# Kernel optimization log

Measured on AMD Instinct MI355X. Metric: run time of the kernel, lower is better.

## Reference

```python
import jax, jax.numpy as jnp
import numpy as np
import math

NUM_HEADS = 8

def setup_inputs() -> dict:
    key = jax.random.key(0)
    ks = jax.random.split(key, 5)
    b, h, w, c = 4, 128, 128, 256
    x = jax.random.normal(ks[0], (b, h, w, c), dtype=jnp.float32)
    scale = 1.0 / math.sqrt(c)  # keep weights reasonably scaled (kaiming-like)
    Wq = jax.random.normal(ks[1], (c, c), dtype=jnp.float32) * scale
    Wk = jax.random.normal(ks[2], (c, c), dtype=jnp.float32) * scale
    Wv = jax.random.normal(ks[3], (c, c), dtype=jnp.float32) * scale
    Wout = jax.random.normal(ks[4], (c, c), dtype=jnp.float32) * scale
    return {"x": x, "Wq": Wq, "Wk": Wk, "Wv": Wv, "Wout": Wout}

def reference(x, Wq, Wk, Wv, Wout):
    b, h, w, c = x.shape
    hw = h * w
    heads = NUM_HEADS
    dh = c // heads
    xs = x.reshape(b, hw, c)
    q = xs @ Wq  # (b, hw, c)
    k = xs @ Wk
    v = xs @ Wv

    def split_heads(t):
        # (b, hw, c) -> (b, c, hw) -> (b, heads, dh, hw)
        return t.transpose(0, 2, 1).reshape(b, heads, dh, hw)

    q = split_heads(q)
    k = split_heads(k)
    v = split_heads(v)
    # L2-normalize along the feature (hw) axis; original has no epsilon
    q = q / jnp.linalg.norm(q, axis=-1, keepdims=True)
    k = k / jnp.linalg.norm(k, axis=-1, keepdims=True)
    d_k = q.shape[-1]  # = hw
    attn = jnp.einsum('bhcd,bhed->bhce', q, k) / math.sqrt(d_k)  # (b,heads,dh,dh)
    attn = jax.nn.softmax(attn, axis=-1)
    vals = jnp.einsum('bhce,bhed->bhcd', attn, v)  # (b,heads,dh,hw)
    vals = vals.transpose(0, 3, 1, 2).reshape(b, hw, c)
    out = (vals @ Wout).reshape(b, h, w, c)
    return out
```

## Files before the change

### kernel.cpp

```cpp
#include <hip/hip_runtime.h>


#define B_   4
#define HW_  16384
#define C_   256

typedef __attribute__((ext_vector_type(8))) short short8;
typedef __attribute__((ext_vector_type(4))) float floatx4;

__device__ __forceinline__ unsigned short f2bf(float f) {
  unsigned u = __builtin_bit_cast(unsigned, f);
  u += 0x7FFFu + ((u >> 16) & 1u);
  return (unsigned short)(u >> 16);
}

__device__ __forceinline__ void gl_lds16(const unsigned short* g, unsigned short* l) {
  __builtin_amdgcn_global_load_lds(
      (const __attribute__((address_space(1))) unsigned int*)g,
      (__attribute__((address_space(3))) unsigned int*)l, 16, 0, 0);
}

__global__ __launch_bounds__(256) void k_cast_tr(const float* __restrict__ x,
                                                 unsigned short* __restrict__ xb,
                                                 unsigned short* __restrict__ xT) {
  __shared__ unsigned short lds[64][72];
  int bid = blockIdx.x;
  int ct = bid & 3;
  int pt = (bid >> 2) & 255;
  int b  = bid >> 10;
  int t = threadIdx.x;
  const float* src = x + ((size_t)(b * HW_ + pt * 64)) * C_ + ct * 64;
#pragma unroll
  for (int e = 0; e < 4; e++) {
    int lin = t + e * 256;
    int p = lin >> 4, c4 = lin & 15;
    float4 v = *(const float4*)(src + (size_t)p * C_ + c4 * 4);
    ushort4 h;
    h.x = f2bf(v.x); h.y = f2bf(v.y); h.z = f2bf(v.z); h.w = f2bf(v.w);
    *(ushort4*)(xb + ((size_t)(b * HW_ + pt * 64 + p)) * C_ + ct * 64 + c4 * 4) = h;
    lds[c4 * 4 + 0][p] = h.x;
    lds[c4 * 4 + 1][p] = h.y;
    lds[c4 * 4 + 2][p] = h.z;
    lds[c4 * 4 + 3][p] = h.w;
  }
  __syncthreads();
#pragma unroll
  for (int e = 0; e < 4; e++) {
    int lin = t + e * 256;
    int c = lin >> 4, p4 = lin & 15;
    ushort4 h;
    h.x = lds[c][p4 * 4 + 0];
    h.y = lds[c][p4 * 4 + 1];
    h.z = lds[c][p4 * 4 + 2];
    h.w = lds[c][p4 * 4 + 3];
    *(ushort4*)(xT + ((size_t)(b * C_ + ct * 64 + c)) * HW_ + pt * 64 + p4 * 4) = h;
  }
}

template <int NST>
__device__ __forceinline__ void nt_loop(const unsigned short* Ab, int lda,
                                        const unsigned short* Bb, int ldb,
                                        unsigned short* At, unsigned short* Bt,
                                        floatx4 acc[4][4]) {
  int t = threadIdx.x;
  int lane = t & 63, w = t >> 6;
  int wm = w >> 1, wn = w & 1;
  int l8 = lane >> 3, l7 = lane & 7;
  int srcoct = l7 ^ l8;
  int l15 = lane & 15, l4 = lane >> 4;
  for (int s = 0; s < NST; s++) {
#pragma unroll
    for (int i = 0; i < 4; i++) {
      int gi = w * 4 + i;
      int row = gi * 8 + l8;
      gl_lds16(Ab + (size_t)row * lda + s * 64 + srcoct * 8, At + gi * 512);
      gl_lds16(Bb + (size_t)row * ldb + s * 64 + srcoct * 8, Bt + gi * 512);
    }
    __syncthreads();
#pragma unroll
    for (int kk = 0; kk < 2; kk++) {
      short8 af[4], bfv[4];
#pragma unroll
      for (int tm = 0; tm < 4; tm++) {
        int row = wm * 64 + tm * 16 + l15;
        int oct = kk * 4 + l4;
        af[tm] = *(const short8*)(At + row * 64 + ((oct ^ (l15 & 7)) * 8));
      }
#pragma unroll
      for (int tn = 0; tn < 4; tn++) {
        int row = wn * 64 + tn * 16 + l15;
        int oct = kk * 4 + l4;
        bfv[tn] = *(const short8*)(Bt + row * 64 + ((oct ^ (l15 & 7)) * 8));
      }
#pragma unroll
      for (int tm = 0; tm < 4; tm++)
#pragma unroll
        for (int tn = 0; tn < 4; tn++)
          acc[tm][tn] = __builtin_amdgcn_mfma_f32_16x16x32_bf16(af[tm], bfv[tn],
                                                                acc[tm][tn], 0, 0, 0);
    }
    __syncthreads();
  }
}

__global__ __launch_bounds__(256) void k_sgemm(const unsigned short* __restrict__ xT,
                                               float* __restrict__ part) {
  __shared__ unsigned short At[128 * 64];
  __shared__ unsigned short Bt[128 * 64];
  int bid = blockIdx.x;
  int ks = bid & 15, nt = (bid >> 4) & 1, mt = (bid >> 5) & 1, b = bid >> 6;
  const unsigned short* Ab = xT + ((size_t)(b * C_ + mt * 128)) * HW_ + ks * 1024;
  const unsigned short* Bb = xT + ((size_t)(b * C_ + nt * 128)) * HW_ + ks * 1024;
  floatx4 acc[4][4];
  floatx4 z = {0.f, 0.f, 0.f, 0.f};
#pragma unroll
  for (int i = 0; i < 4; i++)
#pragma unroll
    for (int j = 0; j < 4; j++) acc[i][j] = z;
  nt_loop<16>(Ab, HW_, Bb, HW_, At, Bt, acc);
  int t = threadIdx.x, lane = t & 63, w = t >> 6;
  int wm = w >> 1, wn = w & 1;
  int l15 = lane & 15, l4 = lane >> 4;
  float* pb = part + ((size_t)((b * 4 + mt * 2 + nt) * 16 + ks)) * 16384;
#pragma unroll
  for (int tm = 0; tm < 4; tm++)
#pragma unroll
    for (int tn = 0; tn < 4; tn++)
#pragma unroll
      for (int r = 0; r < 4; r++) {
        int m = wm * 64 + tm * 16 + l4 * 4 + r;
        int n = wn * 64 + tn * 16 + l15;
        pb[m * 128 + n] = acc[tm][tn][r];
      }
}

__global__ __launch_bounds__(256) void k_sred(const float* __restrict__ part,
                                              float* __restrict__ S) {
  int idx = blockIdx.x * 256 + threadIdx.x;
  int b = idx >> 16;
  int m = (idx >> 8) & 255, n = idx & 255;
  const float* p = part + ((size_t)((b * 4 + (m >> 7) * 2 + (n >> 7)) * 16)) * 16384
                   + (m & 127) * 128 + (n & 127);
  float s = 0.f;
#pragma unroll
  for (int k = 0; k < 16; k++) s += p[k * 16384];
  S[idx] = s;
}

__global__ __launch_bounds__(256) void k_gemm_sw(const float* __restrict__ S,
                                                 const float* __restrict__ Wq,
                                                 const float* __restrict__ Wk,
                                                 float* __restrict__ SWq,
                                                 float* __restrict__ SWk) {
  __shared__ float As[64][17];
  __shared__ float Bs[16][65];
  int bid = blockIdx.x;
  int nt = bid & 7, mt = (bid >> 3) & 3, b = bid >> 5;
  int mb = mt * 64;
  const float* Wsel = (nt < 4) ? Wq : Wk;
  int nb = (nt & 3) * 64;
  int t = threadIdx.x, tx = t & 15, ty = t >> 4;
  float acc[4][4] = {};
  for (int kt = 0; kt < 16; kt++) {
    {
      int row = t >> 2, kq = t & 3;
      float4 v = *(const float4*)(S + ((size_t)(b * C_ + mb + row)) * C_ + kt * 16 + kq * 4);
      As[row][kq * 4 + 0] = v.x; As[row][kq * 4 + 1] = v.y;
      As[row][kq * 4 + 2] = v.z; As[row][kq * 4 + 3] = v.w;
    }
    {
      int kk = t >> 4, n4 = t & 15;
      float4 v = *(const float4*)(Wsel + ((size_t)(kt * 16 + kk)) * C_ + nb + n4 * 4);
      Bs[kk][n4 * 4 + 0] = v.x; Bs[kk][n4 * 4 + 1] = v.y;
      Bs[kk][n4 * 4 + 2] = v.z; Bs[kk][n4 * 4 + 3] = v.w;
    }
    __syncthreads();
#pragma unroll
    for (int k = 0; k < 16; k++) {
      float a[4], bb[4];
#pragma unroll
      for (int i = 0; i < 4; i++) a[i] = As[ty * 4 + i][k];
#pragma unroll
      for (int j = 0; j < 4; j++) bb[j] = Bs[k][tx * 4 + j];
#pragma unroll
      for (int i = 0; i < 4; i++)
#pragma unroll
        for (int j = 0; j < 4; j++) acc[i][j] += a[i] * bb[j];
    }
    __syncthreads();
  }
#pragma unroll
  for (int i = 0; i < 4; i++)
#pragma unroll
    for (int j = 0; j < 4; j++) {
      int row = mb + ty * 4 + i;
      int ng = nt * 64 + tx * 4 + j;
      if (ng < 256) SWq[((size_t)(b * C_ + row)) * C_ + ng] = acc[i][j];
      else          SWk[((size_t)(b * C_ + row)) * C_ + ng - 256] = acc[i][j];
    }
}

__global__ __launch_bounds__(256) void k_gemm_g(const float* __restrict__ Wq,
                                                const float* __restrict__ SWk,
                                                float* __restrict__ Gf) {
  __shared__ float As[64][17];
  __shared__ float Bs[16][65];
  int bid = blockIdx.x;
  int nt = bid & 3, mt = (bid >> 2) & 3, b = bid >> 4;
  int mb = mt * 64, nb = nt * 64;
  int t = threadIdx.x, tx = t & 15, ty = t >> 4;
  float acc[4][4] = {};
  for (int kt = 0; kt < 16; kt++) {
    {
      int kk = t >> 4, m4 = t & 15;
      float4 v = *(const float4*)(Wq + ((size_t)(kt * 16 + kk)) * C_ + mb + m4 * 4);
      As[m4 * 4 + 0][kk] = v.x; As[m4 * 4 + 1][kk] = v.y;
      As[m4 * 4 + 2][kk] = v.z; As[m4 * 4 + 3][kk] = v.w;
    }
    {
      int kk = t >> 4, n4 = t & 15;
      float4 v = *(const float4*)(SWk + ((size_t)(b * C_ + kt * 16 + kk)) * C_ + nb + n4 * 4);
      Bs[kk][n4 * 4 + 0] = v.x; Bs[kk][n4 * 4 + 1] = v.y;
      Bs[kk][n4 * 4 + 2] = v.z; Bs[kk][n4 * 4 + 3] = v.w;
    }
    __syncthreads();
#pragma unroll
    for (int k = 0; k < 16; k++) {
      float a[4], bb[4];
#pragma unroll
      for (int i = 0; i < 4; i++) a[i] = As[ty * 4 + i][k];
#pragma unroll
      for (int j = 0; j < 4; j++) bb[j] = Bs[k][tx * 4 + j];
#pragma unroll
      for (int i = 0; i < 4; i++)
#pragma unroll
        for (int j = 0; j < 4; j++) acc[i][j] += a[i] * bb[j];
    }
    __syncthreads();
  }
#pragma unroll
  for (int i = 0; i < 4; i++)
#pragma unroll
    for (int j = 0; j < 4; j++)
      Gf[((size_t)(b * C_ + mb + ty * 4 + i)) * C_ + nb + tx * 4 + j] = acc[i][j];
}

__global__ __launch_bounds__(256) void k_softmax(const float* __restrict__ Wq,
                                                 const float* __restrict__ Wk,
                                                 const float* __restrict__ SWq,
                                                 const float* __restrict__ SWk,
                                                 const float* __restrict__ Gf,
                                                 float* __restrict__ Aat) {
  __shared__ float qpart[8][32], kpart[8][32], qin[32], kin[32], L[32][33];
  int b = blockIdx.x >> 3, h = blockIdx.x & 7;
  int t = threadIdx.x;
  int i = t & 31, part = t >> 5;
  float s = 0.f;
  for (int k = part * 32; k < part * 32 + 32; k++)
    s += Wq[(size_t)k * C_ + h * 32 + i] * SWq[((size_t)(b * C_ + k)) * C_ + h * 32 + i];
  qpart[part][i] = s;
  s = 0.f;
  for (int k = part * 32; k < part * 32 + 32; k++)
    s += Wk[(size_t)k * C_ + h * 32 + i] * SWk[((size_t)(b * C_ + k)) * C_ + h * 32 + i];
  kpart[part][i] = s;
  __syncthreads();
  if (t < 32) {
    float a = 0.f;
#pragma unroll
    for (int p = 0; p < 8; p++) a += qpart[p][t];
    qin[t] = rsqrtf(a);
  } else if (t < 64) {
    int j = t - 32;
    float a = 0.f;
#pragma unroll
    for (int p = 0; p < 8; p++) a += kpart[p][j];
    kin[j] = rsqrtf(a);
  }
  __syncthreads();
#pragma unroll
  for (int e = 0; e < 4; e++) {
    int idx = t + e * 256;
    int ii = idx >> 5, jj = idx & 31;
    float g = Gf[((size_t)(b * C_ + h * 32 + ii)) * C_ + h * 32 + jj];
    L[ii][jj] = g * qin[ii] * kin[jj] * 0.0078125f;
  }
  __syncthreads();
  if (t < 32) {
    float mx = -1e30f;
#pragma unroll
    for (int j = 0; j < 32; j++) mx = fmaxf(mx, L[t][j]);
    float ex[32];
    float sum = 0.f;
#pragma unroll
    for (int j = 0; j < 32; j++) { ex[j] = __expf(L[t][j] - mx); sum += ex[j]; }
    float inv = 1.0f / sum;
#pragma unroll
    for (int j = 0; j < 32; j++)
      Aat[(((size_t)(b * 8 + h)) * 32 + t) * 32 + j] = ex[j] * inv;
  }
}

__global__ __launch_bounds__(256) void k_attn_t(const float* __restrict__ Aat,
                                                const float* __restrict__ Wout,
                                                float* __restrict__ T) {
  __shared__ float Ah[32][33];
  __shared__ float Wo[32][256];
  int b = blockIdx.x >> 3, h = blockIdx.x & 7;
  int t = threadIdx.x;
#pragma unroll
  for (int e = 0; e < 4; e++) {
    int idx = t + e * 256;
    int ii = idx >> 5, jj = idx & 31;
    Ah[ii][jj] = Aat[(((size_t)(b * 8 + h)) * 32 + ii) * 32 + jj];
  }
#pragma unroll
  for (int r = 0; r < 32; r++) Wo[r][t] = Wout[((size_t)(h * 32 + r)) * C_ + t];
  __syncthreads();
  for (int j = 0; j < 32; j++) {
    float a = 0.f;
#pragma unroll
    for (int i2 = 0; i2 < 32; i2++) a += Ah[i2][j] * Wo[i2][t];
    T[((size_t)(b * C_ + h * 32 + j)) * C_ + t] = a;
  }
}

__global__ __launch_bounds__(256) void k_gemm_w3(const float* __restrict__ Wv,
                                                 const float* __restrict__ T,
                                                 unsigned short* __restrict__ W3bT) {
  __shared__ float As[64][17];
  __shared__ float Bs[16][65];
  int bid = blockIdx.x;
  int nt = bid & 3, mt = (bid >> 2) & 3, b = bid >> 4;
  int mb = mt * 64, nb = nt * 64;
  int t = threadIdx.x, tx = t & 15, ty = t >> 4;
  float acc[4][4] = {};
  for (int kt = 0; kt < 16; kt++) {
    {
      int row = t >> 2, kq = t & 3;
      float4 v = *(const float4*)(Wv + ((size_t)(mb + row)) * C_ + kt * 16 + kq * 4);
      As[row][kq * 4 + 0] = v.x; As[row][kq * 4 + 1] = v.y;
      As[row][kq * 4 + 2] = v.z; As[row][kq * 4 + 3] = v.w;
    }
    {
      int kk = t >> 4, n4 = t & 15;
      float4 v = *(const float4*)(T + ((size_t)(b * C_ + kt * 16 + kk)) * C_ + nb + n4 * 4);
      Bs[kk][n4 * 4 + 0] = v.x; Bs[kk][n4 * 4 + 1] = v.y;
      Bs[kk][n4 * 4 + 2] = v.z; Bs[kk][n4 * 4 + 3] = v.w;
    }
    __syncthreads();
#pragma unroll
    for (int k = 0; k < 16; k++) {
      float a[4], bb[4];
#pragma unroll
      for (int i = 0; i < 4; i++) a[i] = As[ty * 4 + i][k];
#pragma unroll
      for (int j = 0; j < 4; j++) bb[j] = Bs[k][tx * 4 + j];
#pragma unroll
      for (int i = 0; i < 4; i++)
#pragma unroll
        for (int j = 0; j < 4; j++) acc[i][j] += a[i] * bb[j];
    }
    __syncthreads();
  }
#pragma unroll
  for (int i = 0; i < 4; i++)
#pragma unroll
    for (int j = 0; j < 4; j++)
      W3bT[((size_t)(b * C_ + nb + tx * 4 + j)) * C_ + mb + ty * 4 + i] = f2bf(acc[i][j]);
}

__global__ __launch_bounds__(256) void k_out(const unsigned short* __restrict__ xb,
                                             const unsigned short* __restrict__ W3bT,
                                             float* __restrict__ out) {
  __shared__ unsigned short At[128 * 64];
  __shared__ unsigned short Bt[128 * 64];
  int bid = blockIdx.x;
  int ntile = bid & 1, mtile = bid >> 1;
  int b = mtile >> 7;
  const unsigned short* Ab = xb + (size_t)mtile * 128 * C_;
  const unsigned short* Bb = W3bT + ((size_t)(b * C_ + ntile * 128)) * C_;
  floatx4 acc[4][4];
  floatx4 z = {0.f, 0.f, 0.f, 0.f};
#pragma unroll
  for (int i = 0; i < 4; i++)
#pragma unroll
    for (int j = 0; j < 4; j++) acc[i][j] = z;
  nt_loop<4>(Ab, C_, Bb, C_, At, Bt, acc);
  int t = threadIdx.x, lane = t & 63, w = t >> 6;
  int wm = w >> 1, wn = w & 1;
  int l15 = lane & 15, l4 = lane >> 4;
  float* ob = out + (size_t)mtile * 128 * C_ + ntile * 128;
#pragma unroll
  for (int tm = 0; tm < 4; tm++)
#pragma unroll
    for (int tn = 0; tn < 4; tn++)
#pragma unroll
      for (int r = 0; r < 4; r++) {
        int m = wm * 64 + tm * 16 + l4 * 4 + r;
        int n = wn * 64 + tn * 16 + l15;
        ob[(size_t)m * C_ + n] = acc[tm][tn][r];
      }
}

extern "C" void kernel_launch(void* const* d_in, const int* in_sizes, int n_in,
                              void* d_out, int out_size, void* d_ws, size_t ws_size,
                              hipStream_t stream) {
  const float* x    = (const float*)d_in[0];
  const float* Wq   = (const float*)d_in[1];
  const float* Wk   = (const float*)d_in[2];
  const float* Wv   = (const float*)d_in[3];
  const float* Wout = (const float*)d_in[4];
  float* out = (float*)d_out;

  unsigned short* xT = (unsigned short*)d_ws;
  unsigned short* xb = xT + (size_t)16777216;
  float* part = (float*)(xb + (size_t)16777216);
  float* S    = part + (size_t)4194304;
  float* SWq  = S + 262144;
  float* SWk  = SWq + 262144;
  float* Gf   = SWk + 262144;
  float* Aat  = Gf + 262144;
  float* T    = Aat + 32768;
  unsigned short* W3bT = (unsigned short*)(T + 262144);

  k_cast_tr<<<dim3(4096), dim3(256), 0, stream>>>(x, xb, xT);
  k_sgemm<<<dim3(256), dim3(256), 0, stream>>>(xT, part);
  k_sred<<<dim3(1024), dim3(256), 0, stream>>>(part, S);
  k_gemm_sw<<<dim3(128), dim3(256), 0, stream>>>(S, Wq, Wk, SWq, SWk);
  k_gemm_g<<<dim3(64), dim3(256), 0, stream>>>(Wq, SWk, Gf);
  k_softmax<<<dim3(32), dim3(256), 0, stream>>>(Wq, Wk, SWq, SWk, Gf, Aat);
  k_attn_t<<<dim3(32), dim3(256), 0, stream>>>(Aat, Wout, T);
  k_gemm_w3<<<dim3(64), dim3(256), 0, stream>>>(Wv, T, W3bT);
  k_out<<<dim3(1024), dim3(256), 0, stream>>>(xb, W3bT, out);
}
```

Before: 244.6 us.

## Replace split-K reduction with atomics and fuse softmax path into one kernel

The Gram-matrix GEMM now splits K into 32 slices across 512 blocks and accumulates directly into S with float atomicAdd. S is zeroed inside the cast kernel, which removes the partial buffer and the separate reduction kernel. The G, softmax and attention-times-Wout kernels are merged into one per-(batch, head) kernel that stages the weight slices in LDS and computes only the diagonal head block of G. This cuts three launches and several global round-trips, at the cost of atomic contention and a non-deterministic summation order.

```diff
diff --git a/kernel.cpp b/kernel.cpp
--- a/kernel.cpp
+++ b/kernel.cpp
@@ -22,13 +22,18 @@
 
 __global__ __launch_bounds__(256) void k_cast_tr(const float* __restrict__ x,
                                                  unsigned short* __restrict__ xb,
-                                                 unsigned short* __restrict__ xT) {
+                                                 unsigned short* __restrict__ xT,
+                                                 float* __restrict__ S) {
   __shared__ unsigned short lds[64][72];
   int bid = blockIdx.x;
+  int t = threadIdx.x;
+  if (bid < 256) {
+    float4 z = {0.f, 0.f, 0.f, 0.f};
+    ((float4*)S)[bid * 256 + t] = z;
+  }
   int ct = bid & 3;
   int pt = (bid >> 2) & 255;
   int b  = bid >> 10;
-  int t = threadIdx.x;
   const float* src = x + ((size_t)(b * HW_ + pt * 64)) * C_ + ct * 64;
 #pragma unroll
   for (int e = 0; e < 4; e++) {
@@ -104,47 +109,34 @@
 }
 
 __global__ __launch_bounds__(256) void k_sgemm(const unsigned short* __restrict__ xT,
-                                               float* __restrict__ part) {
+                                               float* __restrict__ S) {
   __shared__ unsigned short At[128 * 64];
   __shared__ unsigned short Bt[128 * 64];
   int bid = blockIdx.x;
-  int ks = bid & 15, nt = (bid >> 4) & 1, mt = (bid >> 5) & 1, b = bid >> 6;
-  const unsigned short* Ab = xT + ((size_t)(b * C_ + mt * 128)) * HW_ + ks * 1024;
-  const unsigned short* Bb = xT + ((size_t)(b * C_ + nt * 128)) * HW_ + ks * 1024;
+  int ks = bid & 31, nt = (bid >> 5) & 1, mt = (bid >> 6) & 1, b = bid >> 7;
+  const unsigned short* Ab = xT + ((size_t)(b * C_ + mt * 128)) * HW_ + ks * 512;
+  const unsigned short* Bb = xT + ((size_t)(b * C_ + nt * 128)) * HW_ + ks * 512;
   floatx4 acc[4][4];
   floatx4 z = {0.f, 0.f, 0.f, 0.f};
 #pragma unroll
   for (int i = 0; i < 4; i++)
 #pragma unroll
     for (int j = 0; j < 4; j++) acc[i][j] = z;
-  nt_loop<16>(Ab, HW_, Bb, HW_, At, Bt, acc);
+  nt_loop<8>(Ab, HW_, Bb, HW_, At, Bt, acc);
   int t = threadIdx.x, lane = t & 63, w = t >> 6;
   int wm = w >> 1, wn = w & 1;
   int l15 = lane & 15, l4 = lane >> 4;
-  float* pb = part + ((size_t)((b * 4 + mt * 2 + nt) * 16 + ks)) * 16384;
+  float* Sb = S + (size_t)b * 65536;
 #pragma unroll
   for (int tm = 0; tm < 4; tm++)
 #pragma unroll
     for (int tn = 0; tn < 4; tn++)
 #pragma unroll
       for (int r = 0; r < 4; r++) {
-        int m = wm * 64 + tm * 16 + l4 * 4 + r;
-        int n = wn * 64 + tn * 16 + l15;
-        pb[m * 128 + n] = acc[tm][tn][r];
+        int m = mt * 128 + wm * 64 + tm * 16 + l4 * 4 + r;
+        int n = nt * 128 + wn * 64 + tn * 16 + l15;
+        atomicAdd(Sb + (size_t)m * C_ + n, acc[tm][tn][r]);
       }
-}
-
-__global__ __launch_bounds__(256) void k_sred(const float* __restrict__ part,
-                                              float* __restrict__ S) {
-  int idx = blockIdx.x * 256 + threadIdx.x;
-  int b = idx >> 16;
-  int m = (idx >> 8) & 255, n = idx & 255;
-  const float* p = part + ((size_t)((b * 4 + (m >> 7) * 2 + (n >> 7)) * 16)) * 16384
-                   + (m & 127) * 128 + (n & 127);
-  float s = 0.f;
-#pragma unroll
-  for (int k = 0; k < 16; k++) s += p[k * 16384];
-  S[idx] = s;
 }
 
 __global__ __launch_bounds__(256) void k_gemm_sw(const float* __restrict__ S,
@@ -200,132 +192,92 @@
     }
 }
 
-__global__ __launch_bounds__(256) void k_gemm_g(const float* __restrict__ Wq,
-                                                const float* __restrict__ SWk,
-                                                float* __restrict__ Gf) {
-  __shared__ float As[64][17];
-  __shared__ float Bs[16][65];
-  int bid = blockIdx.x;
-  int nt = bid & 3, mt = (bid >> 2) & 3, b = bid >> 4;
-  int mb = mt * 64, nb = nt * 64;
-  int t = threadIdx.x, tx = t & 15, ty = t >> 4;
-  float acc[4][4] = {};
-  for (int kt = 0; kt < 16; kt++) {
-    {
-      int kk = t >> 4, m4 = t & 15;
-      float4 v = *(const float4*)(Wq + ((size_t)(kt * 16 + kk)) * C_ + mb + m4 * 4);
-      As[m4 * 4 + 0][kk] = v.x; As[m4 * 4 + 1][kk] = v.y;
-      As[m4 * 4 + 2][kk] = v.z; As[m4 * 4 + 3][kk] = v.w;
-    }
-    {
-      int kk = t >> 4, n4 = t & 15;
-      float4 v = *(const float4*)(SWk + ((size_t)(b * C_ + kt * 16 + kk)) * C_ + nb + n4 * 4);
-      Bs[kk][n4 * 4 + 0] = v.x; Bs[kk][n4 * 4 + 1] = v.y;
-      Bs[kk][n4 * 4 + 2] = v.z; Bs[kk][n4 * 4 + 3] = v.w;
-    }
-    __syncthreads();
-#pragma unroll
-    for (int k = 0; k < 16; k++) {
-      float a[4], bb[4];
-#pragma unroll
-      for (int i = 0; i < 4; i++) a[i] = As[ty * 4 + i][k];
-#pragma unroll
-      for (int j = 0; j < 4; j++) bb[j] = Bs[k][tx * 4 + j];
-#pragma unroll
-      for (int i = 0; i < 4; i++)
-#pragma unroll
-        for (int j = 0; j < 4; j++) acc[i][j] += a[i] * bb[j];
-    }
-    __syncthreads();
-  }
-#pragma unroll
-  for (int i = 0; i < 4; i++)
-#pragma unroll
-    for (int j = 0; j < 4; j++)
-      Gf[((size_t)(b * C_ + mb + ty * 4 + i)) * C_ + nb + tx * 4 + j] = acc[i][j];
-}
-
-__global__ __launch_bounds__(256) void k_softmax(const float* __restrict__ Wq,
-                                                 const float* __restrict__ Wk,
-                                                 const float* __restrict__ SWq,
-                                                 const float* __restrict__ SWk,
-                                                 const float* __restrict__ Gf,
-                                                 float* __restrict__ Aat) {
-  __shared__ float qpart[8][32], kpart[8][32], qin[32], kin[32], L[32][33];
+__global__ __launch_bounds__(256) void k_fuse(const float* __restrict__ Wq,
+                                              const float* __restrict__ Wk,
+                                              const float* __restrict__ SWq,
+                                              const float* __restrict__ SWk,
+                                              const float* __restrict__ Wout,
+                                              float* __restrict__ U) {
+  __shared__ float Wqh[256][32];
+  __shared__ float Wkh[256][32];
+  __shared__ float SWqh[256][32];
+  __shared__ float SWkh[256][32];
+  __shared__ float Lg[32][33];
+  __shared__ float qp[8][32], kp[8][32], qin[32], kin[32];
   int b = blockIdx.x >> 3, h = blockIdx.x & 7;
   int t = threadIdx.x;
-  int i = t & 31, part = t >> 5;
-  float s = 0.f;
-  for (int k = part * 32; k < part * 32 + 32; k++)
-    s += Wq[(size_t)k * C_ + h * 32 + i] * SWq[((size_t)(b * C_ + k)) * C_ + h * 32 + i];
-  qpart[part][i] = s;
-  s = 0.f;
-  for (int k = part * 32; k < part * 32 + 32; k++)
-    s += Wk[(size_t)k * C_ + h * 32 + i] * SWk[((size_t)(b * C_ + k)) * C_ + h * 32 + i];
-  kpart[part][i] = s;
+  int col = t & 31, rgrp = t >> 5;
+  for (int r0 = 0; r0 < 256; r0 += 8) {
+    int row = r0 + rgrp;
+    Wqh[row][col]  = Wq[(size_t)row * C_ + h * 32 + col];
+    Wkh[row][col]  = Wk[(size_t)row * C_ + h * 32 + col];
+    SWqh[row][col] = SWq[((size_t)(b * C_ + row)) * C_ + h * 32 + col];
+    SWkh[row][col] = SWk[((size_t)(b * C_ + row)) * C_ + h * 32 + col];
+  }
+  __syncthreads();
+  {
+    float g[4] = {0.f, 0.f, 0.f, 0.f};
+    for (int k = 0; k < 256; k++) {
+      float swk = SWkh[k][col];
+#pragma unroll
+      for (int r = 0; r < 4; r++) g[r] += Wqh[k][rgrp + 8 * r] * swk;
+    }
+#pragma unroll
+    for (int r = 0; r < 4; r++) Lg[rgrp + 8 * r][col] = g[r];
+  }
+  {
+    float sq = 0.f, sk = 0.f;
+    for (int k = rgrp * 32; k < rgrp * 32 + 32; k++) {
+      sq += Wqh[k][col] * SWqh[k][col];
+      sk += Wkh[k][col] * SWkh[k][col];
+    }
+    qp[rgrp][col] = sq;
+    kp[rgrp][col] = sk;
+  }
   __syncthreads();
   if (t < 32) {
     float a = 0.f;
 #pragma unroll
-    for (int p = 0; p < 8; p++) a += qpart[p][t];
+    for (int p = 0; p < 8; p++) a += qp[p][t];
     qin[t] = rsqrtf(a);
   } else if (t < 64) {
     int j = t - 32;
     float a = 0.f;
 #pragma unroll
-    for (int p = 0; p < 8; p++) a += kpart[p][j];
+    for (int p = 0; p < 8; p++) a += kp[p][j];
     kin[j] = rsqrtf(a);
   }
   __syncthreads();
-#pragma unroll
-  for (int e = 0; e < 4; e++) {
-    int idx = t + e * 256;
-    int ii = idx >> 5, jj = idx & 31;
-    float g = Gf[((size_t)(b * C_ + h * 32 + ii)) * C_ + h * 32 + jj];
-    L[ii][jj] = g * qin[ii] * kin[jj] * 0.0078125f;
-  }
-  __syncthreads();
   if (t < 32) {
+    float row[32];
     float mx = -1e30f;
 #pragma unroll
-    for (int j = 0; j < 32; j++) mx = fmaxf(mx, L[t][j]);
-    float ex[32];
+    for (int j = 0; j < 32; j++) {
+      row[j] = Lg[t][j] * qin[t] * kin[j] * 0.0078125f;
+      mx = fmaxf(mx, row[j]);
+    }
     float sum = 0.f;
 #pragma unroll
-    for (int j = 0; j < 32; j++) { ex[j] = __expf(L[t][j] - mx); sum += ex[j]; }
+    for (int j = 0; j < 32; j++) { row[j] = __expf(row[j] - mx); sum += row[j]; }
     float inv = 1.0f / sum;
 #pragma unroll
-    for (int j = 0; j < 32; j++)
-      Aat[(((size_t)(b * 8 + h)) * 32 + t) * 32 + j] = ex[j] * inv;
-  }
-}
-
-__global__ __launch_bounds__(256) void k_attn_t(const float* __restrict__ Aat,
-                                                const float* __restrict__ Wout,
-                                                float* __restrict__ T) {
-  __shared__ float Ah[32][33];
-  __shared__ float Wo[32][256];
-  int b = blockIdx.x >> 3, h = blockIdx.x & 7;
-  int t = threadIdx.x;
-#pragma unroll
-  for (int e = 0; e < 4; e++) {
-    int idx = t + e * 256;
-    int ii = idx >> 5, jj = idx & 31;
-    Ah[ii][jj] = Aat[(((size_t)(b * 8 + h)) * 32 + ii) * 32 + jj];
-  }
+    for (int j = 0; j < 32; j++) Lg[t][j] = row[j] * inv;
+  }
+  __syncthreads();
+  float (*Wo)[256] = reinterpret_cast<float(*)[256]>(&Wqh[0][0]);
 #pragma unroll
   for (int r = 0; r < 32; r++) Wo[r][t] = Wout[((size_t)(h * 32 + r)) * C_ + t];
   __syncthreads();
   for (int j = 0; j < 32; j++) {
     float a = 0.f;
 #pragma unroll
-    for (int i2 = 0; i2 < 32; i2++) a += Ah[i2][j] * Wo[i2][t];
-    T[((size_t)(b * C_ + h * 32 + j)) * C_ + t] = a;
+    for (int i2 = 0; i2 < 32; i2++) a += Lg[i2][j] * Wo[i2][t];
+    U[((size_t)(b * C_ + h * 32 + j)) * C_ + t] = a;
   }
 }
 
 __global__ __launch_bounds__(256) void k_gemm_w3(const float* __restrict__ Wv,
-                                                 const float* __restrict__ T,
+                                                 const float* __restrict__ U,
                                                  unsigned short* __restrict__ W3bT) {
   __shared__ float As[64][17];
   __shared__ float Bs[16][65];
@@ -343,7 +295,7 @@
     }
     {
       int kk = t >> 4, n4 = t & 15;
-      float4 v = *(const float4*)(T + ((size_t)(b * C_ + kt * 16 + kk)) * C_ + nb + n4 * 4);
+      float4 v = *(const float4*)(U + ((size_t)(b * C_ + kt * 16 + kk)) * C_ + nb + n4 * 4);
       Bs[kk][n4 * 4 + 0] = v.x; Bs[kk][n4 * 4 + 1] = v.y;
       Bs[kk][n4 * 4 + 2] = v.z; Bs[kk][n4 * 4 + 3] = v.w;
     }
@@ -414,22 +366,16 @@
 
   unsigned short* xT = (unsigned short*)d_ws;
   unsigned short* xb = xT + (size_t)16777216;
-  float* part = (float*)(xb + (size_t)16777216);
-  float* S    = part + (size_t)4194304;
+  float* S    = (float*)(xb + (size_t)16777216);
   float* SWq  = S + 262144;
   float* SWk  = SWq + 262144;
-  float* Gf   = SWk + 262144;
-  float* Aat  = Gf + 262144;
-  float* T    = Aat + 32768;
-  unsigned short* W3bT = (unsigned short*)(T + 262144);
-
-  k_cast_tr<<<dim3(4096), dim3(256), 0, stream>>>(x, xb, xT);
-  k_sgemm<<<dim3(256), dim3(256), 0, stream>>>(xT, part);
-  k_sred<<<dim3(1024), dim3(256), 0, stream>>>(part, S);
+  float* U    = SWk + 262144;
+  unsigned short* W3bT = (unsigned short*)(U + 262144);
+
+  k_cast_tr<<<dim3(4096), dim3(256), 0, stream>>>(x, xb, xT, S);
+  k_sgemm<<<dim3(512), dim3(256), 0, stream>>>(xT, S);
   k_gemm_sw<<<dim3(128), dim3(256), 0, stream>>>(S, Wq, Wk, SWq, SWk);
-  k_gemm_g<<<dim3(64), dim3(256), 0, stream>>>(Wq, SWk, Gf);
-  k_softmax<<<dim3(32), dim3(256), 0, stream>>>(Wq, Wk, SWq, SWk, Gf, Aat);
-  k_attn_t<<<dim3(32), dim3(256), 0, stream>>>(Aat, Wout, T);
-  k_gemm_w3<<<dim3(64), dim3(256), 0, stream>>>(Wv, T, W3bT);
+  k_fuse<<<dim3(32), dim3(256), 0, stream>>>(Wq, Wk, SWq, SWk, Wout, U);
+  k_gemm_w3<<<dim3(64), dim3(256), 0, stream>>>(Wv, U, W3bT);
   k_out<<<dim3(1024), dim3(256), 0, stream>>>(xb, W3bT, out);
 }
```

After: 240.5 us. About the same (-1.7%).
